# Kernel optimization log

Hardware: AMD Instinct MI355X
Metric: run time of the kernel (lower is better)

## Reference

```python
import jax, jax.numpy as jnp
import numpy as np

HID, HEADS = 2048, 16
HD = HID // HEADS  # head_dim = 128
EPS = 1e-6


def rope_tables(head_dim, max_pos, base=10000.0):
    inv = 1.0 / (base ** (jnp.arange(0, head_dim, 2, dtype=jnp.float32) / head_dim))
    t = jnp.arange(max_pos, dtype=jnp.float32)
    freqs = jnp.outer(t, inv)                      # [max_pos, d/2]
    emb = jnp.concatenate([freqs, freqs], axis=-1)  # [max_pos, d]
    return jnp.cos(emb), jnp.sin(emb)


def rotate_half(x):
    x1, x2 = jnp.split(x, 2, axis=-1)
    return jnp.concatenate([-x2, x1], axis=-1)


def lf_gate(x, c1w, c1b, c2w, c2b, rms_w):
    # x: [b, s, h]; prompt phase -> lf1/lf2 caches are zeros -> zero-pad 1 step on time axis
    xt = jnp.transpose(x, (0, 2, 1))[..., None]                 # [b, h, s, 1]
    xt = jnp.pad(xt, ((0, 0), (0, 0), (1, 0), (0, 0)))           # [b, h, s+1, 1]
    dn = ('NCHW', 'OIHW', 'NCHW')
    o1 = jax.lax.conv_general_dilated(xt, c1w, (1, 1), 'VALID', dimension_numbers=dn)
    o1 = o1 + c1b[None, :, None, None]                           # [b, h/2, s, 1]
    o1 = jnp.pad(o1, ((0, 0), (0, 0), (1, 0), (0, 0)))           # [b, h/2, s+1, 1]
    o2 = jax.lax.conv_general_dilated(o1, c2w, (1, 1), 'VALID', dimension_numbers=dn)
    o2 = o2 + c2b[None, :, None, None]                           # [b, h, s, 1]
    y = jnp.transpose(o2[..., 0], (0, 2, 1)) + x                 # residual, [b, s, h]
    var = jnp.mean(y * y, axis=-1, keepdims=True)
    return y * jax.lax.rsqrt(var + EPS) * rms_w


def setup_inputs() -> dict:
    key = jax.random.key(0)
    ks = jax.random.split(key, 10)
    b, s = 2, 2048
    inp = {
        'hidden_states': jax.random.normal(ks[0], (b, s, HID), jnp.float32),
        'positions': jnp.arange(s, dtype=jnp.int32),
        'wq': jax.random.normal(ks[1], (HID, HID), jnp.float32) * 0.02,
        'wk': jax.random.normal(ks[2], (HID, HID), jnp.float32) * 0.02,
        'wv': jax.random.normal(ks[3], (HID, HID), jnp.float32) * 0.02,
        'wo': jax.random.normal(ks[4], (HID, HID), jnp.float32) * 0.02,
        'conv1_w': jax.random.normal(ks[5], (HID // 2, HID, 2, 1), jnp.float32) * 0.02,
        'conv1_b': jnp.zeros((HID // 2,), jnp.float32),
        'conv2_w': jax.random.normal(ks[6], (HID, HID // 2, 2, 1), jnp.float32) * 0.02,
        'conv2_b': jnp.zeros((HID,), jnp.float32),
        'rms_w': jnp.ones((HID,), jnp.float32),
    }
    return inp


def reference(hidden_states, positions, wq, wk, wv, wo, conv1_w, conv1_b, conv2_w, conv2_b, rms_w):
    b, s, _ = hidden_states.shape
    # value projection from raw hidden states (pre-gate)
    v = (hidden_states @ wv).reshape(b, s, HEADS, HD)            # [b, s, H, d]
    # localized-filtering gate (prompt phase: zero caches)
    h = lf_gate(hidden_states, conv1_w, conv1_b, conv2_w, conv2_b, rms_w)
    q = h @ wq                                                   # [b, s, H*d]
    k = h @ wk
    # faithful Yuan quirk: concat q,k then reshape to [b,s,H,2d] and chunk
    qk = jnp.concatenate([q, k], axis=-1).reshape(b, s, HEADS, 2 * HD)
    q, k = jnp.split(qk, 2, axis=-1)                             # each [b, s, H, d]
    # rotary
    cos, sin = rope_tables(HD, 8192)
    c = cos[positions][None, :, None, :]                         # [1, s, 1, d]
    sn = sin[positions][None, :, None, :]
    q = q * c + rotate_half(q) * sn
    k = k * c + rotate_half(k) * sn
    # causal attention (paged attention reduces to this for the prompt)
    scale = HD ** -0.5
    scores = jnp.einsum('bqhd,bkhd->bhqk', q, k) * scale         # [b, H, s, s]
    mask = jnp.tril(jnp.ones((s, s), dtype=bool))
    scores = jnp.where(mask[None, None], scores, jnp.finfo(scores.dtype).min)
    probs = jax.nn.softmax(scores, axis=-1)
    out = jnp.einsum('bhqk,bkhd->bqhd', probs, v).reshape(b, s, HEADS * HD)
    return out @ wo
```

## Files before the change

### kernel.cpp

```cpp
#include <hip/hip_runtime.h>

#define HID 2048
#define HEADS 16
#define HD 128
#define BATCH 2
#define S 2048
#define ROWS (BATCH*S)

typedef short short8 __attribute__((ext_vector_type(8)));
typedef unsigned short ushort4v __attribute__((ext_vector_type(4)));
typedef unsigned short ushort2v __attribute__((ext_vector_type(2)));
typedef float f32x4 __attribute__((ext_vector_type(4)));
typedef __bf16 bf16x8 __attribute__((ext_vector_type(8)));
typedef __bf16 bf16x4 __attribute__((ext_vector_type(4)));

static __device__ __forceinline__ float b2f(unsigned short u) {
  union { float f; unsigned int i; } v; v.i = ((unsigned int)u) << 16; return v.f;
}
static __device__ __forceinline__ unsigned short f2b(float f) {
  union { float f; unsigned int i; } v; v.f = f;
  unsigned int u = v.i;
  unsigned int r = ((u >> 16) & 1u) + 0x7fffu;
  return (unsigned short)((u + r) >> 16);
}

static __device__ __forceinline__ void gload_lds16(const unsigned short* g, unsigned short* l) {
  __builtin_amdgcn_global_load_lds(
      (const __attribute__((address_space(1))) unsigned int*)(const void*)g,
      (__attribute__((address_space(3))) unsigned int*)(void*)l,
      16, 0, 0);
}

__global__ void fill_debug(unsigned short* __restrict__ out, long n) {
  long i = (long)blockIdx.x * blockDim.x + threadIdx.x;
  if (i < n) out[i] = 0x447A;
}

__global__ void prep_all(const float* __restrict__ c1w, const float* __restrict__ c2w,
                         const float* __restrict__ x, const int* __restrict__ positions,
                         const float* __restrict__ c1b, const float* __restrict__ c2b,
                         const float* __restrict__ rmsw,
                         unsigned short* __restrict__ w1t0, unsigned short* __restrict__ w1t1,
                         unsigned short* __restrict__ w2t0, unsigned short* __restrict__ w2t1,
                         unsigned short* __restrict__ xb,
                         float* __restrict__ ctab, float* __restrict__ stab,
                         unsigned short* __restrict__ c1bb, unsigned short* __restrict__ c2bb,
                         unsigned short* __restrict__ rmswb, unsigned short* __restrict__ zpg) {
  int job = blockIdx.y;
  if (job == 0 || job == 1) {
    const float* w = (job == 0) ? c1w : c2w;
    unsigned short* o0 = (job == 0) ? w1t0 : w2t0;
    unsigned short* o1 = (job == 0) ? w1t1 : w2t1;
    long i = (long)blockIdx.x * 256 + threadIdx.x;
    f32x4 v = *(const f32x4*)(w + i*4);
    ushort2v a = { f2b(v[0]), f2b(v[2]) };
    ushort2v b = { f2b(v[1]), f2b(v[3]) };
    *(ushort2v*)(o0 + i*2) = a;
    *(ushort2v*)(o1 + i*2) = b;
  } else if (job == 2) {
    long i = (long)blockIdx.x * 256 + threadIdx.x;
    #pragma unroll
    for (int rep = 0; rep < 2; ++rep) {
      long idx = i + (long)rep * 1048576L;
      f32x4 v = *(const f32x4*)(x + idx*4);
      ushort4v o = { f2b(v[0]), f2b(v[1]), f2b(v[2]), f2b(v[3]) };
      *(ushort4v*)(xb + idx*4) = o;
    }
  } else {
    int bx = blockIdx.x;
    if (bx < 512) {
      int t = bx * 4 + (threadIdx.x >> 6);
      int i = threadIdx.x & 63;
      float pos = (float)positions[t];
      float inv = powf(10000.0f, -(float)i / 64.0f);
      float ang = pos * inv;
      float sv, cv;
      sincosf(ang, &sv, &cv);
      ctab[t*64 + i] = cv;
      stab[t*64 + i] = sv;
    } else if (bx < 544) {
      int i = (bx - 512) * 256 + threadIdx.x;
      if (i < 1024) c1bb[i] = f2b(c1b[i]);
      if (i < 2048) { c2bb[i] = f2b(c2b[i]); rmswb[i] = f2b(rmsw[i]); }
      zpg[i] = 0;
    }
  }
}

__global__ void transpose4(const float* __restrict__ s0, const float* __restrict__ s1,
                           const float* __restrict__ s2, const float* __restrict__ s3,
                           unsigned short* __restrict__ d0, unsigned short* __restrict__ d1,
                           unsigned short* __restrict__ d2, unsigned short* __restrict__ d3) {
  __shared__ unsigned short tl[64][73];
  const float* in; unsigned short* out; int perm;
  switch (blockIdx.z) {
    case 0:  in = s0; out = d0; perm = 1; break;
    case 1:  in = s1; out = d1; perm = 1; break;
    case 2:  in = s2; out = d2; perm = 0; break;
    default: in = s3; out = d3; perm = 0; break;
  }
  int n0 = blockIdx.x * 64, k0 = blockIdx.y * 64;
  int tid = threadIdx.x;
  int r = tid >> 3, c8 = (tid & 7) * 8;
  #pragma unroll
  for (int j = 0; j < 2; ++j) {
    int rr = r + j*32;
    const float* p = in + (size_t)(k0 + rr)*HID + n0 + c8;
    f32x4 v0 = *(const f32x4*)p;
    f32x4 v1 = *(const f32x4*)(p + 4);
    #pragma unroll
    for (int e = 0; e < 4; ++e) { tl[rr][c8 + e] = f2b(v0[e]); tl[rr][c8 + 4 + e] = f2b(v1[e]); }
  }
  __syncthreads();
  #pragma unroll
  for (int j = 0; j < 2; ++j) {
    int rr = r + j*32;
    int orow = n0 + rr;
    if (perm) {
      int s5 = (orow >> 5) & 3;
      s5 = (s5 == 1) ? 2 : (s5 == 2) ? 1 : s5;
      orow = (orow & ~127) | (s5 << 5) | (orow & 31);
    }
    short8 v;
    #pragma unroll
    for (int e = 0; e < 8; ++e) v[e] = (short)tl[c8 + e][rr];
    *(short8*)(out + (size_t)orow*HID + k0 + c8) = v;
  }
}


struct SPtrs { const unsigned short* p[6]; };

static __device__ __forceinline__ void build_ptrs(SPtrs& sp,
    const unsigned short* Ap, const unsigned short* Bp, int Ksz, int sh,
    int m0, int n0, const unsigned short* zpg, int tid) {
  int lane = tid & 63;
  int scol = (((lane & 7) * 16) ^ (((lane >> 3) & 7) << 4)) >> 1;
  #pragma unroll
  for (int j = 0; j < 2; ++j) {
    int row = ((tid >> 6) * 2 + j) * 8 + (lane >> 3);
    int gr = m0 + row;
    sp.p[j]     = (sh && ((gr & (S - 1)) == 0)) ? (zpg + scol)
                                                : (Ap + (size_t)(gr - sh)*Ksz + scol);
    sp.p[2 + j] = Bp + (size_t)(n0 + row)*Ksz + scol;
    sp.p[4 + j] = Bp + (size_t)(n0 + 128 + row)*Ksz + scol;
  }
}

static __device__ __forceinline__ void stage6(unsigned short* buf, SPtrs& sp, int tid) {
  int c0 = (tid >> 6) * 1024;
  gload_lds16(sp.p[0], buf + c0);
  gload_lds16(sp.p[1], buf + c0 + 512);
  gload_lds16(sp.p[2], buf + 8192  + c0);
  gload_lds16(sp.p[3], buf + 8192  + c0 + 512);
  gload_lds16(sp.p[4], buf + 16384 + c0);
  gload_lds16(sp.p[5], buf + 16384 + c0 + 512);
  #pragma unroll
  for (int i = 0; i < 6; ++i) sp.p[i] += 64;
}

static __device__ __forceinline__ void rd_af(const unsigned short* Ah, bf16x8 (&afr)[4][2],
                                             int wm, int lr, int col0, int axor) {
  #pragma unroll
  for (int mi = 0; mi < 4; ++mi) {
    const unsigned short* rp = Ah + (wm*64 + mi*16 + lr) * 64;
    #pragma unroll
    for (int kk = 0; kk < 2; ++kk)
      afr[mi][kk] = *(const bf16x8*)(rp + (((kk*64 + col0) ^ axor) >> 1));
  }
}
static __device__ __forceinline__ void rd_bf(const unsigned short* Bh, bf16x8 (&bfr)[2][2],
                                             int wn, int lr, int col0, int axor) {
  #pragma unroll
  for (int ni = 0; ni < 2; ++ni) {
    const unsigned short* rp = Bh + (wn*32 + ni*16 + lr) * 64;
    #pragma unroll
    for (int kk = 0; kk < 2; ++kk)
      bfr[ni][kk] = *(const bf16x8*)(rp + (((kk*64 + col0) ^ axor) >> 1));
  }
}
static __device__ __forceinline__ void mfma16(const bf16x8 (&afr)[4][2], const bf16x8 (&bfr)[2][2],
                                              f32x4 (&ac)[4][2]) {
  #pragma unroll
  for (int kk = 0; kk < 2; ++kk)
    #pragma unroll
    for (int mi = 0; mi < 4; ++mi)
      #pragma unroll
      for (int ni = 0; ni < 2; ++ni)
        ac[mi][ni] = __builtin_amdgcn_mfma_f32_16x16x32_bf16(afr[mi][kk], bfr[ni][kk], ac[mi][ni], 0, 0, 0);
}

static __device__ __forceinline__ void gemm8_core(
    unsigned short* lds,
    const unsigned short* __restrict__ A1, const unsigned short* __restrict__ A2,
    const unsigned short* __restrict__ B1, const unsigned short* __restrict__ B2,
    int K1, int K2,
    const unsigned short* __restrict__ bias, const unsigned short* __restrict__ resid,
    void* __restrict__ Cout, int outmode, int N, int m0, int n0,
    int a1shift, const unsigned short* __restrict__ zrow) {
  int tid = threadIdx.x;
  int lane = tid & 63, w = tid >> 6;
  int wm = w >> 2, wn = w & 3;
  int lr = lane & 15, g = lane >> 4;
  int col0 = g * 16;
  int axor = (lr & 7) << 4;
  int nk1 = K1 >> 6;
  int nk = (K1 + K2) >> 6;
  f32x4 acc[2][4][2] = {};
  bf16x8 afr[4][2], bfr0[2][2], bfr1[2][2];

  unsigned short* buf0 = lds;
  unsigned short* buf1 = lds + 24576;
  unsigned short* buf2 = lds + 49152;

  SPtrs sp;
  build_ptrs(sp, A1, B1, K1, a1shift, m0, n0, zrow, tid);

  stage6(buf0, sp, tid);
  stage6(buf1, sp, tid);

  unsigned short* cur = buf0;
  unsigned short* nx1 = buf1;
  unsigned short* nx2 = buf2;
  for (int t = 0; t < nk; ++t) {
    if (t < nk - 1) asm volatile("s_waitcnt vmcnt(6)" ::: "memory");
    else            asm volatile("s_waitcnt vmcnt(0)" ::: "memory");
    __builtin_amdgcn_s_barrier();
    asm volatile("" ::: "memory");

    rd_af(cur,         afr,  wm, lr, col0, axor);
    rd_bf(cur + 8192,  bfr0, wn, lr, col0, axor);
    rd_bf(cur + 16384, bfr1, wn, lr, col0, axor);
    if (t + 2 < nk) {
      if (t + 2 == nk1) build_ptrs(sp, A2, B2, K2, 0, m0, n0, zrow, tid);
      stage6(nx2, sp, tid);
    }
    __builtin_amdgcn_s_setprio(1);
    mfma16(afr, bfr0, acc[0]);
    mfma16(afr, bfr1, acc[1]);
    __builtin_amdgcn_s_setprio(0);

    unsigned short* tmp = cur; cur = nx1; nx1 = nx2; nx2 = tmp;
  }

  #pragma unroll
  for (int qn = 0; qn < 2; ++qn)
    #pragma unroll
    for (int mi = 0; mi < 4; ++mi) {
      int row0 = m0 + wm*64 + mi*16 + g*4;
      #pragma unroll
      for (int ni = 0; ni < 2; ++ni) {
        int col = n0 + qn*128 + wn*32 + ni*16 + lr;
        float bv = bias ? b2f(bias[col]) : 0.f;
        f32x4 a = acc[qn][mi][ni];
        if (outmode == 3) {
          int bb = row0 >> 11;
          int s0 = row0 & (S - 1);
          size_t base = ((size_t)bb * HID + col) * S + s0;
          ushort4v pk;
          #pragma unroll
          for (int j = 0; j < 4; ++j) pk[j] = f2b(a[j]);
          *(ushort4v*)((unsigned short*)Cout + base) = pk;
        } else {
          #pragma unroll
          for (int j = 0; j < 4; ++j) {
            size_t idx = (size_t)(row0 + j) * N + col;
            float v = a[j] + bv;
            if (resid) v += b2f(resid[idx]);
            if (outmode == 1) ((float*)Cout)[idx] = v;
            else ((unsigned short*)Cout)[idx] = f2b(v);
          }
        }
      }
    }
}

template<int SHIFT>
__launch_bounds__(512, 1)
__global__ void gemm8_bt(const unsigned short* __restrict__ A1,
                         const unsigned short* __restrict__ A2,
                         const unsigned short* __restrict__ B1,
                         const unsigned short* __restrict__ B2,
                         int K1, int K2,
                         const unsigned short* __restrict__ bias,
                         const unsigned short* __restrict__ resid,
                         void* __restrict__ Cout, int outmode, int N,
                         const unsigned short* __restrict__ zrow) {
  __shared__ __align__(16) unsigned short lds[73728];
  gemm8_core(lds, A1, A2, B1, B2, K1, K2, bias, resid, Cout, outmode, N,
             blockIdx.x*128, blockIdx.y*256, SHIFT, zrow);
}

struct GemmJob {
  const unsigned short *A1, *A2, *B1, *B2;
  int K1, K2;
  const unsigned short *bias;
  void* Cout; int outmode; int N; int nby; int a1shift;
};

__launch_bounds__(512, 1)
__global__ void gemm8_dual(GemmJob j0, GemmJob j1, const unsigned short* __restrict__ zrow) {
  __shared__ __align__(16) unsigned short lds[73728];
  int by = blockIdx.y;
  GemmJob j;
  if (by < j0.nby) { j = j0; } else { j = j1; by -= j0.nby; }
  gemm8_core(lds, j.A1, j.A2, j.B1, j.B2, j.K1, j.K2, j.bias, nullptr,
             j.Cout, j.outmode, j.N, blockIdx.x*128, by*256, j.a1shift, zrow);
}


struct HPtr { const unsigned short* p0; const unsigned short* p1; };
static __device__ __forceinline__ void hinit(HPtr& h, const unsigned short* base,
                                             int row0, int tid) {
  int lane = tid & 63;
  int scol = (((lane & 7) * 16) ^ (((lane >> 3) & 7) << 4)) >> 1;
  int r0 = ((tid >> 6) * 2) * 8 + (lane >> 3);
  h.p0 = base + (size_t)(row0 + r0) * 2048 + scol;
  h.p1 = base + (size_t)(row0 + r0 + 8) * 2048 + scol;
}
static __device__ __forceinline__ void hstage(unsigned short* slot, HPtr& h, int tid) {
  int c0 = (tid >> 6) * 1024;
  gload_lds16(h.p0, slot + c0);
  gload_lds16(h.p1, slot + c0 + 512);
  h.p0 += 64; h.p1 += 64;
}

__launch_bounds__(512, 1)
__global__ void gemm256_bt(const unsigned short* __restrict__ A,
                           const unsigned short* __restrict__ B,
                           unsigned short* __restrict__ C, int N) {
  __shared__ __align__(16) unsigned short lds[65536];
  int tid = threadIdx.x;
  int lane = tid & 63, w = tid >> 6;
  int wm = w >> 2, wn = w & 3;
  int lr = lane & 15, g = lane >> 4;
  int col0 = g * 16;
  int axor = (lr & 7) << 4;
  int m0 = blockIdx.x * 256, n0 = blockIdx.y * 256;
  const int nk = 2048 >> 6;
  f32x4 acc[2][2][4][2] = {};
  bf16x8 af[4][2], bf0[2][2], bf1[2][2];

  HPtr hA0, hA1, hB0, hB1;
  hinit(hA0, A, m0,       tid);
  hinit(hA1, A, m0 + 128, tid);
  hinit(hB0, B, n0,       tid);
  hinit(hB1, B, n0 + 128, tid);

  hstage(lds + 0,             hA0, tid);
  hstage(lds + 8192,          hA1, tid);
  hstage(lds + 16384,         hB0, tid);
  hstage(lds + 24576,         hB1, tid);
  hstage(lds + 32768 + 0,     hA0, tid);
  hstage(lds + 32768 + 16384, hB0, tid);
  hstage(lds + 32768 + 24576, hB1, tid);
  asm volatile("s_waitcnt vmcnt(6)" ::: "memory");
  __builtin_amdgcn_s_barrier();
  asm volatile("" ::: "memory");

  for (int t = 0; t < nk; ++t) {
    unsigned short* cur = lds + (t & 1) * 32768;
    unsigned short* oth = lds + ((t & 1) ^ 1) * 32768;

    rd_af(cur,         af,  wm, lr, col0, axor);
    rd_bf(cur + 16384, bf0, wn, lr, col0, axor);
    if (t + 1 < nk) hstage(oth + 8192, hA1, tid);
    __builtin_amdgcn_s_barrier();
    asm volatile("s_waitcnt lgkmcnt(0)" ::: "memory");
    __builtin_amdgcn_s_setprio(1);
    mfma16(af, bf0, acc[0][0]);
    __builtin_amdgcn_s_setprio(0);
    __builtin_amdgcn_s_barrier();

    rd_bf(cur + 24576, bf1, wn, lr, col0, axor);
    if (t + 2 < nk) hstage(cur, hA0, tid);
    __builtin_amdgcn_s_barrier();
    asm volatile("s_waitcnt lgkmcnt(0)" ::: "memory");
    __builtin_amdgcn_s_setprio(1);
    mfma16(af, bf1, acc[0][1]);
    __builtin_amdgcn_s_setprio(0);
    __builtin_amdgcn_s_barrier();

    rd_af(cur + 8192, af, wm, lr, col0, axor);
    if (t + 2 < nk) hstage(cur + 16384, hB0, tid);
    __builtin_amdgcn_s_barrier();
    asm volatile("s_waitcnt lgkmcnt(0)" ::: "memory");
    __builtin_amdgcn_s_setprio(1);
    mfma16(af, bf1, acc[1][1]);
    __builtin_amdgcn_s_setprio(0);
    __builtin_amdgcn_s_barrier();

    if (t + 2 < nk) hstage(cur + 24576, hB1, tid);
    __builtin_amdgcn_s_barrier();
    asm volatile("s_waitcnt lgkmcnt(0)" ::: "memory");
    __builtin_amdgcn_s_setprio(1);
    mfma16(af, bf0, acc[1][0]);
    __builtin_amdgcn_s_setprio(0);
    if (t + 2 < nk) asm volatile("s_waitcnt vmcnt(6)" ::: "memory");
    else            asm volatile("s_waitcnt vmcnt(0)" ::: "memory");
    __builtin_amdgcn_s_barrier();
    asm volatile("" ::: "memory");
  }

  #pragma unroll
  for (int qm = 0; qm < 2; ++qm)
    #pragma unroll
    for (int mi = 0; mi < 4; ++mi) {
      int row0 = m0 + qm*128 + wm*64 + mi*16 + g*4;
      #pragma unroll
      for (int qn = 0; qn < 2; ++qn)
        #pragma unroll
        for (int ni = 0; ni < 2; ++ni) {
          int col = n0 + qn*128 + wn*32 + ni*16 + lr;
          f32x4 a = acc[qm][qn][mi][ni];
          #pragma unroll
          for (int j = 0; j < 4; ++j)
            C[(size_t)(row0 + j) * N + col] = f2b(a[j]);
        }
    }
}

__global__ void rmsnorm_rows(const unsigned short* __restrict__ y,
                             const unsigned short* __restrict__ w,
                             unsigned short* __restrict__ out) {
  int r = blockIdx.x;
  int c8 = threadIdx.x * 8;
  const unsigned short* yr = y + (size_t)r * HID;
  short8 v = *(const short8*)(yr + c8);
  float f[8];
  float ss = 0.f;
  #pragma unroll
  for (int e = 0; e < 8; ++e) { f[e] = b2f((unsigned short)v[e]); ss += f[e]*f[e]; }
  #pragma unroll
  for (int o = 32; o; o >>= 1) ss += __shfl_xor(ss, o);
  __shared__ float red[4];
  if ((threadIdx.x & 63) == 0) red[threadIdx.x >> 6] = ss;
  __syncthreads();
  float tot = red[0] + red[1] + red[2] + red[3];
  float scale = rsqrtf(tot / (float)HID + 1e-6f);
  short8 wv = *(const short8*)(w + c8);
  short8 o8;
  #pragma unroll
  for (int e = 0; e < 8; ++e) o8[e] = (short)f2b(f[e] * scale * b2f((unsigned short)wv[e]));
  *(short8*)(out + (size_t)r*HID + c8) = o8;
}

__global__ void rope_rearrange(const unsigned short* __restrict__ qkf,
                               const float* __restrict__ ctab, const float* __restrict__ stab,
                               unsigned short* __restrict__ qr, unsigned short* __restrict__ kr) {
  int r = blockIdx.x;
  int t = r & (S - 1);
  int h = threadIdx.x >> 4;
  int i4 = (threadIdx.x & 15) * 4;
  int pc = (i4 & 31) + ((i4 >> 5) << 6);
  const unsigned short* qk = qkf + (size_t)r * (2*HID) + h * 256;
  f32x4 c = *(const f32x4*)(ctab + t*64 + i4);
  f32x4 s = *(const f32x4*)(stab + t*64 + i4);
  ushort4v q1 = *(const ushort4v*)(qk + pc);
  ushort4v q2 = *(const ushort4v*)(qk + pc + 32);
  ushort4v k1 = *(const ushort4v*)(qk + 128 + pc);
  ushort4v k2 = *(const ushort4v*)(qk + 128 + pc + 32);
  size_t o = (size_t)r * HID + (size_t)h * HD;
  const float SC = 0.08838834764831845f * 1.44269504088896340f;
  ushort4v oq1, oq2, ok1, ok2;
  #pragma unroll
  for (int e = 0; e < 4; ++e) {
    float a = b2f(q1[e]), b = b2f(q2[e]);
    float x = b2f(k1[e]), y = b2f(k2[e]);
    oq1[e] = f2b((a*c[e] - b*s[e]) * SC);
    oq2[e] = f2b((b*c[e] + a*s[e]) * SC);
    ok1[e] = f2b(x*c[e] - y*s[e]);
    ok2[e] = f2b(y*c[e] + x*s[e]);
  }
  *(ushort4v*)(qr + o + i4)      = oq1;
  *(ushort4v*)(qr + o + 64 + i4) = oq2;
  *(ushort4v*)(kr + o + i4)      = ok1;
  *(ushort4v*)(kr + o + 64 + i4) = ok2;
}

#define KT 64

static __device__ __forceinline__ void attn_pass(
    int qt, int b, int h, unsigned short* lds,
    const unsigned short* __restrict__ Qr, const unsigned short* __restrict__ Kr,
    const unsigned short* __restrict__ Vt, unsigned short* __restrict__ Out) {
  int tid = threadIdx.x, lane = tid & 63, w = tid >> 6;
  int q0 = qt * 64;
  size_t bS = (size_t)b * S;
  size_t ho = (size_t)h * HD;
  int lr = lane & 15, g = lane >> 4;
  int rsw = (lane & 7) << 3;
  __syncthreads();
  bf16x8 bq[4];
  {
    int qrow = q0 + w*16 + lr;
    const unsigned short* qp = Qr + (bS + qrow)*HID + ho + g*8;
    #pragma unroll
    for (int kk = 0; kk < 4; ++kk) bq[kk] = *(const bf16x8*)(qp + kk*32);
  }
  const unsigned short* kp[4];
  const unsigned short* vp[4];
  #pragma unroll
  for (int j = 0; j < 4; ++j) {
    int c = w*4 + j;
    int rk = c*4 + (lane >> 4);
    int sck = ((lane & 15) * 8) ^ ((rk & 7) << 3);
    kp[j] = Kr + (bS + rk)*HID + ho + sck;
    int rv = c*8 + (lane >> 3);
    int scv = ((lane & 7) * 8) ^ ((rv & 7) << 3);
    vp[j] = Vt + ((size_t)b*HID + ho + rv)*S + scv;
  }
  int cdst = (w*4) * 512;
  unsigned short* curK = lds;
  unsigned short* curV = lds + 8192;
  unsigned short* nxtK = lds + 16384;
  unsigned short* nxtV = lds + 24576;
  #pragma unroll
  for (int j = 0; j < 4; ++j) {
    gload_lds16(kp[j], curK + cdst + j*512);
    gload_lds16(vp[j], curV + cdst + j*512);
    kp[j] += (size_t)KT * HID;
    vp[j] += KT;
  }
  f32x4 o[8] = {};
  float m = -1e30f, l = 0.f;
  unsigned short* PlW = lds + 32768 + w*1024;
  int ntiles = qt + 1;
  for (int kt = 0; kt < ntiles; ++kt) {
    asm volatile("s_waitcnt vmcnt(0)" ::: "memory");
    __builtin_amdgcn_s_barrier();
    asm volatile("" ::: "memory");
    if (kt + 1 < ntiles) {
      #pragma unroll
      for (int j = 0; j < 4; ++j) {
        gload_lds16(kp[j], nxtK + cdst + j*512);
        gload_lds16(vp[j], nxtV + cdst + j*512);
        kp[j] += (size_t)KT * HID;
        vp[j] += KT;
      }
    }
    f32x4 st[4] = {};
    __builtin_amdgcn_s_setprio(1);
    #pragma unroll
    for (int kk = 0; kk < 4; ++kk) {
      #pragma unroll
      for (int mi = 0; mi < 4; ++mi) {
        bf16x8 a = *(const bf16x8*)(&curK[(mi*16 + lr)*128 + ((kk*32 + g*8) ^ rsw)]);
        st[mi] = __builtin_amdgcn_mfma_f32_16x16x32_bf16(a, bq[kk], st[mi], 0, 0, 0);
      }
    }
    __builtin_amdgcn_s_setprio(0);
    bool lastt = (kt == ntiles - 1);
    float tm = -1e30f;
    #pragma unroll
    for (int mi = 0; mi < 4; ++mi)
      #pragma unroll
      for (int r = 0; r < 4; ++r) {
        float v = st[mi][r];
        if (lastt && (mi*16 + 4*g + r) > (w*16 + lr)) v = -1e30f;
        st[mi][r] = v;
        tm = fmaxf(tm, v);
      }
    tm = fmaxf(tm, __shfl_xor(tm, 16));
    tm = fmaxf(tm, __shfl_xor(tm, 32));
    if (!__all(tm - m <= 11.5f)) {
      float mn = fmaxf(m, tm);
      float sc = exp2f(m - mn);
      float s0 = __shfl(sc, 4*g+0), s1 = __shfl(sc, 4*g+1);
      float s2 = __shfl(sc, 4*g+2), s3 = __shfl(sc, 4*g+3);
      #pragma unroll
      for (int ni = 0; ni < 8; ++ni) {
        o[ni][0] *= s0; o[ni][1] *= s1; o[ni][2] *= s2; o[ni][3] *= s3;
      }
      l *= sc;
      m = mn;
    }
    float ts = 0.f;
    __bf16 pbf[4][4];
    #pragma unroll
    for (int mi = 0; mi < 4; ++mi)
      #pragma unroll
      for (int r = 0; r < 4; ++r) {
        float p = exp2f(st[mi][r] - m);
        ts += p;
        pbf[mi][r] = (__bf16)p;
      }
    ts += __shfl_xor(ts, 16);
    ts += __shfl_xor(ts, 32);
    l += ts;
    #pragma unroll
    for (int mi = 0; mi < 4; ++mi) {
      bf16x4 pk = { pbf[mi][0], pbf[mi][1], pbf[mi][2], pbf[mi][3] };
      *(bf16x4*)(&PlW[lr*64 + ((mi*16 + 4*g) ^ rsw)]) = pk;
    }
    asm volatile("" ::: "memory");
    __builtin_amdgcn_s_setprio(1);
    #pragma unroll
    for (int kk = 0; kk < 2; ++kk) {
      int pc = (kk*32 + g*8) ^ rsw;
      bf16x8 a = *(const bf16x8*)(&PlW[lr*64 + pc]);
      #pragma unroll
      for (int ni = 0; ni < 8; ++ni) {
        bf16x8 bv = *(const bf16x8*)(&curV[(ni*16 + lr)*64 + pc]);
        o[ni] = __builtin_amdgcn_mfma_f32_16x16x32_bf16(a, bv, o[ni], 0, 0, 0);
      }
    }
    __builtin_amdgcn_s_setprio(0);
    unsigned short* t0 = curK; curK = nxtK; nxtK = t0;
    unsigned short* t1 = curV; curV = nxtV; nxtV = t1;
  }
  float l0 = __shfl(l, 4*g+0), l1 = __shfl(l, 4*g+1);
  float l2 = __shfl(l, 4*g+2), l3 = __shfl(l, 4*g+3);
  float i0 = 1.f/l0, i1 = 1.f/l1, i2 = 1.f/l2, i3 = 1.f/l3;
  int rbase = q0 + w*16 + 4*g;
  #pragma unroll
  for (int ni = 0; ni < 8; ++ni) {
    size_t cbase = ho + ni*16 + lr;
    Out[(bS + rbase + 0)*HID + cbase] = f2b(o[ni][0]*i0);
    Out[(bS + rbase + 1)*HID + cbase] = f2b(o[ni][1]*i1);
    Out[(bS + rbase + 2)*HID + cbase] = f2b(o[ni][2]*i2);
    Out[(bS + rbase + 3)*HID + cbase] = f2b(o[ni][3]*i3);
  }
}

__launch_bounds__(256, 2)
__global__ void attn_mfma(const unsigned short* __restrict__ Qr,
                          const unsigned short* __restrict__ Kr,
                          const unsigned short* __restrict__ Vt,
                          unsigned short* __restrict__ Out) {
  __shared__ __align__(16) unsigned short lds[36864];
  int bh = blockIdx.x;
  int b = bh >> 4, h = bh & 15;
  int by = blockIdx.y;
  attn_pass(31 - by, b, h, lds, Qr, Kr, Vt, Out);
  attn_pass(by,      b, h, lds, Qr, Kr, Vt, Out);
}

extern "C" void kernel_launch(void* const* d_in, const int* in_sizes, int n_in,
                              void* d_out, int out_size, void* d_ws, size_t ws_size,
                              hipStream_t stream) {
  const float* x_raw   = (const float*)d_in[0];
  const int* positions = (const int*)d_in[1];
  const float* wq_raw  = (const float*)d_in[2];
  const float* wk_raw  = (const float*)d_in[3];
  const float* wv_raw  = (const float*)d_in[4];
  const float* wo_raw  = (const float*)d_in[5];
  const float* c1w_raw = (const float*)d_in[6];
  const float* c1b_raw = (const float*)d_in[7];
  const float* c2w_raw = (const float*)d_in[8];
  const float* c2b_raw = (const float*)d_in[9];
  const float* rms_raw = (const float*)d_in[10];

  const size_t WS_NEEDED = 140000000;
  if (ws_size < WS_NEEDED) {
    long n = (long)out_size;
    fill_debug<<<dim3((unsigned)((n + 255) / 256)), dim3(256), 0, stream>>>((unsigned short*)d_out, n);
    return;
  }

  char* ws = (char*)d_ws;
  size_t off = 0;
  auto alloc = [&](size_t bytes) { char* p = ws + off; off += (bytes + 255) & ~(size_t)255; return p; };
  float* ctab          = (float*)alloc((size_t)S*64*4);
  float* stab          = (float*)alloc((size_t)S*64*4);
  unsigned short* wqkt = (unsigned short*)alloc((size_t)2*HID*HID*2);
  unsigned short* wvt  = (unsigned short*)alloc((size_t)HID*HID*2);
  unsigned short* wot  = (unsigned short*)alloc((size_t)HID*HID*2);
  unsigned short* w1t0 = (unsigned short*)alloc((size_t)1024*HID*2);
  unsigned short* w1t1 = (unsigned short*)alloc((size_t)1024*HID*2);
  unsigned short* w2t0 = (unsigned short*)alloc((size_t)HID*1024*2);
  unsigned short* w2t1 = (unsigned short*)alloc((size_t)HID*1024*2);
  unsigned short* xb   = (unsigned short*)alloc((size_t)ROWS*HID*2);
  unsigned short* qrb  = (unsigned short*)alloc((size_t)ROWS*HID*2);
  unsigned short* o1   = (unsigned short*)alloc((size_t)ROWS*1024*2);
  unsigned short* yb   = (unsigned short*)alloc((size_t)ROWS*HID*2);
  unsigned short* hg   = (unsigned short*)alloc((size_t)ROWS*HID*2);
  unsigned short* qkf  = (unsigned short*)alloc((size_t)ROWS*2*HID*2);
  unsigned short* vtg  = (unsigned short*)alloc((size_t)BATCH*HID*S*2);
  unsigned short* c1bb = (unsigned short*)alloc(1024*2);
  unsigned short* c2bb = (unsigned short*)alloc(2048*2);
  unsigned short* rmswb= (unsigned short*)alloc(2048*2);
  unsigned short* zpg  = (unsigned short*)alloc(8192*2);
  unsigned short* krr  = xb;
  unsigned short* attn = yb;

  dim3 b256(256);
  dim3 b512(512);
  prep_all<<<dim3(4096, 4), b256, 0, stream>>>(c1w_raw, c2w_raw, x_raw, positions,
                                               c1b_raw, c2b_raw, rms_raw,
                                               w1t0, w1t1, w2t0, w2t1, xb,
                                               ctab, stab, c1bb, c2bb, rmswb, zpg);
  transpose4<<<dim3(32,32,4), b256, 0, stream>>>(wq_raw, wk_raw, wv_raw, wo_raw,
                                                 wqkt, wqkt + (size_t)HID*HID, wvt, wot);
  {
    GemmJob j0 = { xb, xb, w1t0, w1t1, HID, HID, c1bb, o1, 0, 1024, 4, 1 };
    GemmJob j1 = { xb, xb, wvt,  wvt,  HID, 0,   nullptr, vtg, 3, HID, 8, 0 };
    gemm8_dual<<<dim3(ROWS/128, 12), b512, 0, stream>>>(j0, j1, zpg);
  }
  gemm8_bt<1><<<dim3(ROWS/128, HID/256), b512, 0, stream>>>(o1, o1, w2t0, w2t1, 1024, 1024, c2bb, xb, yb, 0, HID, zpg);
  rmsnorm_rows<<<dim3(ROWS), b256, 0, stream>>>(yb, rmswb, hg);
  gemm256_bt<<<dim3(ROWS/256, (2*HID)/256), b512, 0, stream>>>(hg, wqkt, qkf, 2*HID);
  rope_rearrange<<<dim3(ROWS), b256, 0, stream>>>(qkf, ctab, stab, qrb, krr);
  attn_mfma<<<dim3(BATCH*HEADS, 16), b256, 0, stream>>>(qrb, krr, vtg, attn);
  gemm8_bt<0><<<dim3(ROWS/128, HID/256), b512, 0, stream>>>(attn, attn, wot, wot, HID, 0, nullptr, nullptr, d_out, 1, HID, nullptr);
}
```

Baseline: 355.4 us.

## Transpose GEMM tile to 256x128 with half-staged double-buffered LDS pipeline

The shared GEMM core moves from a 128x256 tile (M x N) with a three-slot LDS ring to a 256x128 tile. Each K step is split into two halves: the second A half-tile for the next step is loaded while the first half's MFMAs run, and the next-next first half plus B are loaded during the second half's MFMAs. LDS use drops from 144KB to 96KB, and the grid becomes 16 x N/128. The new schedule adds more barriers per K step and reloads A fragments between the halves, which may cost throughput.

```diff
diff --git a/kernel.cpp b/kernel.cpp
--- a/kernel.cpp
+++ b/kernel.cpp
@@ -129,71 +129,75 @@
 }
 
 
-struct SPtrs { const unsigned short* p[6]; };
-
-static __device__ __forceinline__ void build_ptrs(SPtrs& sp,
-    const unsigned short* Ap, const unsigned short* Bp, int Ksz, int sh,
-    int m0, int n0, const unsigned short* zpg, int tid) {
+static __device__ __forceinline__ int swz_scol(int lane) {
+  return (((lane & 7) * 16) ^ (((lane >> 3) & 7) << 4)) >> 1;
+}
+
+static __device__ __forceinline__ void rd_af(const unsigned short* Ah, bf16x8 (&afr)[4][2],
+                                             int wm, int lr, int col0, int axor) {
+  #pragma unroll
+  for (int mi = 0; mi < 4; ++mi) {
+    const unsigned short* rp = Ah + (wm*64 + mi*16 + lr) * 64;
+    #pragma unroll
+    for (int kk = 0; kk < 2; ++kk)
+      afr[mi][kk] = *(const bf16x8*)(rp + (((kk*64 + col0) ^ axor) >> 1));
+  }
+}
+static __device__ __forceinline__ void rd_bf(const unsigned short* Bh, bf16x8 (&bfr)[2][2],
+                                             int wn, int lr, int col0, int axor) {
+  #pragma unroll
+  for (int ni = 0; ni < 2; ++ni) {
+    const unsigned short* rp = Bh + (wn*32 + ni*16 + lr) * 64;
+    #pragma unroll
+    for (int kk = 0; kk < 2; ++kk)
+      bfr[ni][kk] = *(const bf16x8*)(rp + (((kk*64 + col0) ^ axor) >> 1));
+  }
+}
+static __device__ __forceinline__ void mfma16(const bf16x8 (&afr)[4][2], const bf16x8 (&bfr)[2][2],
+                                              f32x4 (&ac)[4][2]) {
+  #pragma unroll
+  for (int kk = 0; kk < 2; ++kk)
+    #pragma unroll
+    for (int mi = 0; mi < 4; ++mi)
+      #pragma unroll
+      for (int ni = 0; ni < 2; ++ni)
+        ac[mi][ni] = __builtin_amdgcn_mfma_f32_16x16x32_bf16(afr[mi][kk], bfr[ni][kk], ac[mi][ni], 0, 0, 0);
+}
+
+static __device__ __forceinline__ void bld_A(const unsigned short** p, const unsigned short* Ap,
+    int Ksz, int sh, int mbase, const unsigned short* zpg, int tid) {
   int lane = tid & 63;
-  int scol = (((lane & 7) * 16) ^ (((lane >> 3) & 7) << 4)) >> 1;
+  int scol = swz_scol(lane);
   #pragma unroll
   for (int j = 0; j < 2; ++j) {
     int row = ((tid >> 6) * 2 + j) * 8 + (lane >> 3);
-    int gr = m0 + row;
-    sp.p[j]     = (sh && ((gr & (S - 1)) == 0)) ? (zpg + scol)
-                                                : (Ap + (size_t)(gr - sh)*Ksz + scol);
-    sp.p[2 + j] = Bp + (size_t)(n0 + row)*Ksz + scol;
-    sp.p[4 + j] = Bp + (size_t)(n0 + 128 + row)*Ksz + scol;
-  }
-}
-
-static __device__ __forceinline__ void stage6(unsigned short* buf, SPtrs& sp, int tid) {
+    int gr = mbase + row;
+    p[j] = (sh && ((gr & (S - 1)) == 0)) ? (zpg + scol)
+                                         : (Ap + (size_t)(gr - sh)*Ksz + scol);
+  }
+}
+static __device__ __forceinline__ void bld_B(const unsigned short** p, const unsigned short* Bp,
+    int Ksz, int nbase, int tid) {
+  int lane = tid & 63;
+  int scol = swz_scol(lane);
+  #pragma unroll
+  for (int j = 0; j < 2; ++j) {
+    int row = ((tid >> 6) * 2 + j) * 8 + (lane >> 3);
+    p[j] = Bp + (size_t)(nbase + row)*Ksz + scol;
+  }
+}
+static __device__ __forceinline__ void st_half(unsigned short* slot, const unsigned short** p, int tid) {
   int c0 = (tid >> 6) * 1024;
-  gload_lds16(sp.p[0], buf + c0);
-  gload_lds16(sp.p[1], buf + c0 + 512);
-  gload_lds16(sp.p[2], buf + 8192  + c0);
-  gload_lds16(sp.p[3], buf + 8192  + c0 + 512);
-  gload_lds16(sp.p[4], buf + 16384 + c0);
-  gload_lds16(sp.p[5], buf + 16384 + c0 + 512);
-  #pragma unroll
-  for (int i = 0; i < 6; ++i) sp.p[i] += 64;
-}
-
-static __device__ __forceinline__ void rd_af(const unsigned short* Ah, bf16x8 (&afr)[4][2],
-                                             int wm, int lr, int col0, int axor) {
-  #pragma unroll
-  for (int mi = 0; mi < 4; ++mi) {
-    const unsigned short* rp = Ah + (wm*64 + mi*16 + lr) * 64;
-    #pragma unroll
-    for (int kk = 0; kk < 2; ++kk)
-      afr[mi][kk] = *(const bf16x8*)(rp + (((kk*64 + col0) ^ axor) >> 1));
-  }
-}
-static __device__ __forceinline__ void rd_bf(const unsigned short* Bh, bf16x8 (&bfr)[2][2],
-                                             int wn, int lr, int col0, int axor) {
-  #pragma unroll
-  for (int ni = 0; ni < 2; ++ni) {
-    const unsigned short* rp = Bh + (wn*32 + ni*16 + lr) * 64;
-    #pragma unroll
-    for (int kk = 0; kk < 2; ++kk)
-      bfr[ni][kk] = *(const bf16x8*)(rp + (((kk*64 + col0) ^ axor) >> 1));
-  }
-}
-static __device__ __forceinline__ void mfma16(const bf16x8 (&afr)[4][2], const bf16x8 (&bfr)[2][2],
-                                              f32x4 (&ac)[4][2]) {
-  #pragma unroll
-  for (int kk = 0; kk < 2; ++kk)
-    #pragma unroll
-    for (int mi = 0; mi < 4; ++mi)
-      #pragma unroll
-      for (int ni = 0; ni < 2; ++ni)
-        ac[mi][ni] = __builtin_amdgcn_mfma_f32_16x16x32_bf16(afr[mi][kk], bfr[ni][kk], ac[mi][ni], 0, 0, 0);
-}
-
-static __device__ __forceinline__ void gemm8_core(
+  gload_lds16(p[0], slot + c0);
+  gload_lds16(p[1], slot + c0 + 512);
+  p[0] += 64; p[1] += 64;
+}
+
+
+static __device__ __forceinline__ void gemm128_core(
     unsigned short* lds,
-    const unsigned short* __restrict__ A1, const unsigned short* __restrict__ A2,
-    const unsigned short* __restrict__ B1, const unsigned short* __restrict__ B2,
+    const unsigned short* __restrict__ A1s, const unsigned short* __restrict__ A2s,
+    const unsigned short* __restrict__ B1s, const unsigned short* __restrict__ B2s,
     int K1, int K2,
     const unsigned short* __restrict__ bias, const unsigned short* __restrict__ resid,
     void* __restrict__ Cout, int outmode, int N, int m0, int n0,
@@ -207,52 +211,68 @@
   int nk1 = K1 >> 6;
   int nk = (K1 + K2) >> 6;
   f32x4 acc[2][4][2] = {};
-  bf16x8 afr[4][2], bfr0[2][2], bfr1[2][2];
-
-  unsigned short* buf0 = lds;
-  unsigned short* buf1 = lds + 24576;
-  unsigned short* buf2 = lds + 49152;
-
-  SPtrs sp;
-  build_ptrs(sp, A1, B1, K1, a1shift, m0, n0, zrow, tid);
-
-  stage6(buf0, sp, tid);
-  stage6(buf1, sp, tid);
-
-  unsigned short* cur = buf0;
-  unsigned short* nx1 = buf1;
-  unsigned short* nx2 = buf2;
+  bf16x8 af[4][2], bf[2][2];
+
+  const unsigned short* pA0[2];
+  const unsigned short* pA1[2];
+  const unsigned short* pB[2];
+  bld_A(pA0, A1s, K1, a1shift, m0,       zrow, tid);
+  bld_A(pA1, A1s, K1, a1shift, m0 + 128, zrow, tid);
+  bld_B(pB,  B1s, K1, n0, tid);
+
+  st_half(lds + 0,     pA0, tid);
+  st_half(lds + 8192,  pA1, tid);
+  st_half(lds + 16384, pB,  tid);
+  st_half(lds + 24576 + 0,     pA0, tid);
+  st_half(lds + 24576 + 16384, pB,  tid);
+  asm volatile("s_waitcnt vmcnt(4)" ::: "memory");
+  __builtin_amdgcn_s_barrier();
+  asm volatile("" ::: "memory");
+
   for (int t = 0; t < nk; ++t) {
-    if (t < nk - 1) asm volatile("s_waitcnt vmcnt(6)" ::: "memory");
+    unsigned short* cur = lds + (t & 1) * 24576;
+    unsigned short* oth = lds + ((t & 1) ^ 1) * 24576;
+
+    rd_af(cur,         af, wm, lr, col0, axor);
+    rd_bf(cur + 16384, bf, wn, lr, col0, axor);
+    if (t + 1 < nk) {
+      if (t + 1 == nk1) bld_A(pA1, A2s, K2, 0, m0 + 128, zrow, tid);
+      st_half(oth + 8192, pA1, tid);
+    }
+    __builtin_amdgcn_s_barrier();
+    asm volatile("s_waitcnt lgkmcnt(0)" ::: "memory");
+    __builtin_amdgcn_s_setprio(1);
+    mfma16(af, bf, acc[0]);
+    __builtin_amdgcn_s_setprio(0);
+    __builtin_amdgcn_s_barrier();
+
+    rd_af(cur + 8192, af, wm, lr, col0, axor);
+    if (t + 2 < nk) {
+      if (t + 2 == nk1) { bld_A(pA0, A2s, K2, 0, m0, zrow, tid); bld_B(pB, B2s, K2, n0, tid); }
+      st_half(cur,         pA0, tid);
+      st_half(cur + 16384, pB,  tid);
+    }
+    __builtin_amdgcn_s_barrier();
+    asm volatile("s_waitcnt lgkmcnt(0)" ::: "memory");
+    __builtin_amdgcn_s_setprio(1);
+    mfma16(af, bf, acc[1]);
+    __builtin_amdgcn_s_setprio(0);
+    if (t + 2 < nk) asm volatile("s_waitcnt vmcnt(4)" ::: "memory");
     else            asm volatile("s_waitcnt vmcnt(0)" ::: "memory");
     __builtin_amdgcn_s_barrier();
     asm volatile("" ::: "memory");
-
-    rd_af(cur,         afr,  wm, lr, col0, axor);
-    rd_bf(cur + 8192,  bfr0, wn, lr, col0, axor);
-    rd_bf(cur + 16384, bfr1, wn, lr, col0, axor);
-    if (t + 2 < nk) {
-      if (t + 2 == nk1) build_ptrs(sp, A2, B2, K2, 0, m0, n0, zrow, tid);
-      stage6(nx2, sp, tid);
-    }
-    __builtin_amdgcn_s_setprio(1);
-    mfma16(afr, bfr0, acc[0]);
-    mfma16(afr, bfr1, acc[1]);
-    __builtin_amdgcn_s_setprio(0);
-
-    unsigned short* tmp = cur; cur = nx1; nx1 = nx2; nx2 = tmp;
-  }
-
-  #pragma unroll
-  for (int qn = 0; qn < 2; ++qn)
+  }
+
+  #pragma unroll
+  for (int qm = 0; qm < 2; ++qm)
     #pragma unroll
     for (int mi = 0; mi < 4; ++mi) {
-      int row0 = m0 + wm*64 + mi*16 + g*4;
+      int row0 = m0 + qm*128 + wm*64 + mi*16 + g*4;
       #pragma unroll
       for (int ni = 0; ni < 2; ++ni) {
-        int col = n0 + qn*128 + wn*32 + ni*16 + lr;
+        int col = n0 + wn*32 + ni*16 + lr;
         float bv = bias ? b2f(bias[col]) : 0.f;
-        f32x4 a = acc[qn][mi][ni];
+        f32x4 a = acc[qm][mi][ni];
         if (outmode == 3) {
           int bb = row0 >> 11;
           int s0 = row0 & (S - 1);
@@ -277,18 +297,18 @@
 
 template<int SHIFT>
 __launch_bounds__(512, 1)
-__global__ void gemm8_bt(const unsigned short* __restrict__ A1,
-                         const unsigned short* __restrict__ A2,
-                         const unsigned short* __restrict__ B1,
-                         const unsigned short* __restrict__ B2,
-                         int K1, int K2,
-                         const unsigned short* __restrict__ bias,
-                         const unsigned short* __restrict__ resid,
-                         void* __restrict__ Cout, int outmode, int N,
-                         const unsigned short* __restrict__ zrow) {
-  __shared__ __align__(16) unsigned short lds[73728];
-  gemm8_core(lds, A1, A2, B1, B2, K1, K2, bias, resid, Cout, outmode, N,
-             blockIdx.x*128, blockIdx.y*256, SHIFT, zrow);
+__global__ void gemm128_bt(const unsigned short* __restrict__ A1,
+                           const unsigned short* __restrict__ A2,
+                           const unsigned short* __restrict__ B1,
+                           const unsigned short* __restrict__ B2,
+                           int K1, int K2,
+                           const unsigned short* __restrict__ bias,
+                           const unsigned short* __restrict__ resid,
+                           void* __restrict__ Cout, int outmode, int N,
+                           const unsigned short* __restrict__ zrow) {
+  __shared__ __align__(16) unsigned short lds[49152];
+  gemm128_core(lds, A1, A2, B1, B2, K1, K2, bias, resid, Cout, outmode, N,
+               blockIdx.x*256, blockIdx.y*128, SHIFT, zrow);
 }
 
 struct GemmJob {
@@ -299,21 +319,20 @@
 };
 
 __launch_bounds__(512, 1)
-__global__ void gemm8_dual(GemmJob j0, GemmJob j1, const unsigned short* __restrict__ zrow) {
-  __shared__ __align__(16) unsigned short lds[73728];
+__global__ void gemm128_dual(GemmJob j0, GemmJob j1, const unsigned short* __restrict__ zrow) {
+  __shared__ __align__(16) unsigned short lds[49152];
   int by = blockIdx.y;
   GemmJob j;
   if (by < j0.nby) { j = j0; } else { j = j1; by -= j0.nby; }
-  gemm8_core(lds, j.A1, j.A2, j.B1, j.B2, j.K1, j.K2, j.bias, nullptr,
-             j.Cout, j.outmode, j.N, blockIdx.x*128, by*256, j.a1shift, zrow);
-}
-
+  gemm128_core(lds, j.A1, j.A2, j.B1, j.B2, j.K1, j.K2, j.bias, nullptr,
+               j.Cout, j.outmode, j.N, blockIdx.x*256, by*128, j.a1shift, zrow);
+}
 
 struct HPtr { const unsigned short* p0; const unsigned short* p1; };
 static __device__ __forceinline__ void hinit(HPtr& h, const unsigned short* base,
                                              int row0, int tid) {
   int lane = tid & 63;
-  int scol = (((lane & 7) * 16) ^ (((lane >> 3) & 7) << 4)) >> 1;
+  int scol = swz_scol(lane);
   int r0 = ((tid >> 6) * 2) * 8 + (lane >> 3);
   h.p0 = base + (size_t)(row0 + r0) * 2048 + scol;
   h.p1 = base + (size_t)(row0 + r0 + 8) * 2048 + scol;
@@ -693,14 +712,14 @@
   transpose4<<<dim3(32,32,4), b256, 0, stream>>>(wq_raw, wk_raw, wv_raw, wo_raw,
                                                  wqkt, wqkt + (size_t)HID*HID, wvt, wot);
   {
-    GemmJob j0 = { xb, xb, w1t0, w1t1, HID, HID, c1bb, o1, 0, 1024, 4, 1 };
-    GemmJob j1 = { xb, xb, wvt,  wvt,  HID, 0,   nullptr, vtg, 3, HID, 8, 0 };
-    gemm8_dual<<<dim3(ROWS/128, 12), b512, 0, stream>>>(j0, j1, zpg);
-  }
-  gemm8_bt<1><<<dim3(ROWS/128, HID/256), b512, 0, stream>>>(o1, o1, w2t0, w2t1, 1024, 1024, c2bb, xb, yb, 0, HID, zpg);
+    GemmJob j0 = { xb, xb, w1t0, w1t1, HID, HID, c1bb, o1, 0, 1024, 8, 1 };
+    GemmJob j1 = { xb, xb, wvt,  wvt,  HID, 0,   nullptr, vtg, 3, HID, 16, 0 };
+    gemm128_dual<<<dim3(ROWS/256, 24), b512, 0, stream>>>(j0, j1, zpg);
+  }
+  gemm128_bt<1><<<dim3(ROWS/256, HID/128), b512, 0, stream>>>(o1, o1, w2t0, w2t1, 1024, 1024, c2bb, xb, yb, 0, HID, zpg);
   rmsnorm_rows<<<dim3(ROWS), b256, 0, stream>>>(yb, rmswb, hg);
   gemm256_bt<<<dim3(ROWS/256, (2*HID)/256), b512, 0, stream>>>(hg, wqkt, qkf, 2*HID);
   rope_rearrange<<<dim3(ROWS), b256, 0, stream>>>(qkf, ctab, stab, qrb, krr);
   attn_mfma<<<dim3(BATCH*HEADS, 16), b256, 0, stream>>>(qrb, krr, vtg, attn);
-  gemm8_bt<0><<<dim3(ROWS/128, HID/256), b512, 0, stream>>>(attn, attn, wot, wot, HID, 0, nullptr, nullptr, d_out, 1, HID, nullptr);
-}
+  gemm128_bt<0><<<dim3(ROWS/256, HID/128), b512, 0, stream>>>(attn, attn, wot, wot, HID, 0, nullptr, nullptr, d_out, 1, HID, nullptr);
+}
```

Result: slower. 373.1 us (+5.0%).
